# Optimization experiments

Measured on AMD Instinct MI355X. Metric: run time of the kernel, lower is better.

## Reference

```python
import jax, jax.numpy as jnp
import numpy as np

EPS = 1e-12  # matches torch F.normalize eps


def _l2_normalize(x, axis=-1):
    # torch.F.normalize: x / max(||x||, eps)
    n = jnp.sqrt(jnp.sum(x * x, axis=axis, keepdims=True))
    return x / jnp.maximum(n, EPS)


def setup_inputs() -> dict:
    N, n_classes, embed_dim = 32768, 1000, 1024
    key = jax.random.key(0)
    k_feat, k_lab, k_proto = jax.random.split(key, 3)

    features = jax.random.normal(k_feat, (N, embed_dim), dtype=jnp.float32)

    # one-hot float labels, as expected by `torch.matmul(labels, self.mean_class)`
    y = jax.random.randint(k_lab, (N,), 0, n_classes)
    labels = jax.nn.one_hot(y, n_classes, dtype=jnp.float32)

    # predefined prototypes: orthonormal rows (ortho_group.rvs equivalent via QR)
    g = jax.random.normal(k_proto, (embed_dim, embed_dim), dtype=jnp.float32)
    q, _ = jnp.linalg.qr(g)
    mean_class = q[:n_classes]  # [n_classes, embed_dim], orthonormal rows

    return {"features": features, "labels": labels, "mean_class": mean_class}


def reference(features, labels, mean_class):
    # features: [N, D]; labels: [N, C] one-hot; mean_class: [C, D]
    # (3-D feature mean-pooling branch not exercised: inputs are 2-D)
    proto_y = labels @ mean_class                 # [N, D]
    f = _l2_normalize(features, axis=1)
    p = _l2_normalize(proto_y, axis=1)
    # diag(f @ p.T) == rowwise dot product -> same math, O(N*D) not O(N^2*D)
    cos = jnp.einsum("nd,nd->n", f, p)            # [N]
    return jnp.mean(1.0 - cos)
```

## Files before the change

### kernel.cpp

```cpp
#include <hip/hip_runtime.h>

constexpr int N_CLASSES = 1000;
constexpr int EMBED     = 1024;

typedef float floatx4 __attribute__((ext_vector_type(4)));

__device__ __forceinline__ floatx4 ntload(const floatx4* p) {
    return __builtin_nontemporal_load(p);
}

__global__ __launch_bounds__(256, 4) void angular_pipelined_kernel(
    const float* __restrict__ features,
    const float* __restrict__ labels,
    const float* __restrict__ mean_class,
    float* __restrict__ partials,
    int n_rows)
{
    const int tid  = threadIdx.x;
    const int lane = tid & 63;
    const int wave = tid >> 6;
    const int wave_id = (blockIdx.x * blockDim.x + tid) >> 6;
    const int n_waves = (gridDim.x * blockDim.x) >> 6;

    float acc = 0.0f;

    int r = wave_id;
    floatx4 f0, f1, f2, f3, l0, l1, l2, l3;
    if (r < n_rows) {
        const floatx4* frow = (const floatx4*)(features + (size_t)r * EMBED);
        f0 = ntload(frow + lane);       f1 = ntload(frow + lane + 64);
        f2 = ntload(frow + lane + 128); f3 = ntload(frow + lane + 192);
        const floatx4* lrow = (const floatx4*)(labels + (size_t)r * N_CLASSES);
        l0 = ntload(lrow + lane);       l1 = ntload(lrow + lane + 64);
        l2 = ntload(lrow + lane + 128);
        l3 = (lane < N_CLASSES / 4 - 192) ? ntload(lrow + lane + 192)
                                          : (floatx4){0.f, 0.f, 0.f, 0.f};
    }

    while (r < n_rows) {
        const int rn = r + n_waves;
        const bool has_next = rn < n_rows;
        floatx4 nf0, nf1, nf2, nf3, nl0, nl1, nl2, nl3;
        if (has_next) {
            const floatx4* frow = (const floatx4*)(features + (size_t)rn * EMBED);
            nf0 = ntload(frow + lane);       nf1 = ntload(frow + lane + 64);
            nf2 = ntload(frow + lane + 128); nf3 = ntload(frow + lane + 192);
            const floatx4* lrow = (const floatx4*)(labels + (size_t)rn * N_CLASSES);
            nl0 = ntload(lrow + lane);       nl1 = ntload(lrow + lane + 64);
            nl2 = ntload(lrow + lane + 128);
            nl3 = (lane < N_CLASSES / 4 - 192) ? ntload(lrow + lane + 192)
                                               : (floatx4){0.f, 0.f, 0.f, 0.f};
        }

        int cand = -1;
        #define SCAN(V, IDX) { \
            if (V.x != 0.f || V.y != 0.f || V.z != 0.f || V.w != 0.f) { \
                int c_ = 4 * (IDX); \
                if      (V.y != 0.f) c_ += 1; \
                else if (V.z != 0.f) c_ += 2; \
                else if (V.w != 0.f) c_ += 3; \
                cand = c_; \
            } }
        SCAN(l0, lane) SCAN(l1, lane + 64) SCAN(l2, lane + 128) SCAN(l3, lane + 192)
        #undef SCAN

        unsigned long long m = __ballot(cand >= 0);
        int cls = __shfl(cand, __ffsll(m) - 1, 64);
        cls = __builtin_amdgcn_readfirstlane(cls);

        const floatx4* prow = (const floatx4*)(mean_class + (size_t)cls * EMBED);
        floatx4 p0 = prow[lane];
        floatx4 p1 = prow[lane + 64];
        floatx4 p2 = prow[lane + 128];
        floatx4 p3 = prow[lane + 192];

        float ff = 0.f, pp = 0.f, fp = 0.f;
        #define DOT3(F, P) \
            ff += F.x*F.x + F.y*F.y + F.z*F.z + F.w*F.w; \
            pp += P.x*P.x + P.y*P.y + P.z*P.z + P.w*P.w; \
            fp += F.x*P.x + F.y*P.y + F.z*P.z + F.w*P.w;
        DOT3(f0, p0) DOT3(f1, p1) DOT3(f2, p2) DOT3(f3, p3)
        #undef DOT3

        #pragma unroll
        for (int msk = 1; msk < 64; msk <<= 1) {
            ff += __shfl_xor(ff, msk, 64);
            pp += __shfl_xor(pp, msk, 64);
            fp += __shfl_xor(fp, msk, 64);
        }
        acc += 1.0f - fp / (fmaxf(sqrtf(ff), 1e-12f) * fmaxf(sqrtf(pp), 1e-12f));

        r = rn;
        if (has_next) {
            f0 = nf0; f1 = nf1; f2 = nf2; f3 = nf3;
            l0 = nl0; l1 = nl1; l2 = nl2; l3 = nl3;
        }
    }

    __shared__ float s_red[4];
    if (lane == 0) s_red[wave] = acc;
    __syncthreads();
    if (tid == 0)
        partials[blockIdx.x] = s_red[0] + s_red[1] + s_red[2] + s_red[3];
}

__global__ __launch_bounds__(256) void reduce_partials_kernel(
    const float* __restrict__ partials, int num_partials,
    float* __restrict__ out, float inv_n)
{
    const int tid  = threadIdx.x;
    const int lane = tid & 63;
    const int wave = tid >> 6;
    __shared__ float s_red[4];

    float acc = 0.0f;
    for (int i = tid; i < num_partials; i += 256)
        acc += partials[i];
    #pragma unroll
    for (int msk = 1; msk < 64; msk <<= 1)
        acc += __shfl_xor(acc, msk, 64);
    if (lane == 0) s_red[wave] = acc;
    __syncthreads();
    if (tid == 0)
        out[0] = (s_red[0] + s_red[1] + s_red[2] + s_red[3]) * inv_n;
}

extern "C" void kernel_launch(void* const* d_in, const int* in_sizes, int n_in,
                              void* d_out, int out_size, void* d_ws, size_t ws_size,
                              hipStream_t stream) {
    const float* features   = (const float*)d_in[0];
    const float* labels     = (const float*)d_in[1];
    const float* mean_class = (const float*)d_in[2];
    float* out = (float*)d_out;
    float* partials = (float*)d_ws;

    const int n_rows = in_sizes[0] / EMBED;
    const int num_blocks = 1024;

    angular_pipelined_kernel<<<num_blocks, 256, 0, stream>>>(
        features, labels, mean_class, partials, n_rows);
    reduce_partials_kernel<<<1, 256, 0, stream>>>(
        partials, num_blocks, out, 1.0f / (float)n_rows);
}
```

Measured before the change: 256.0 us.

## Split label scan into separate kernel and simplify feature dot pass

```diff
diff --git a/kernel.cpp b/kernel.cpp
--- a/kernel.cpp
+++ b/kernel.cpp
@@ -9,12 +9,43 @@
     return __builtin_nontemporal_load(p);
 }
 
-__global__ __launch_bounds__(256, 4) void angular_pipelined_kernel(
+__global__ __launch_bounds__(256, 8) void label_scan_kernel(
+    const float* __restrict__ labels,
+    int* __restrict__ cls_arr, int n_rows)
+{
+    const int tid  = threadIdx.x;
+    const int lane = tid & 63;
+    const int wave_id = (blockIdx.x * blockDim.x + tid) >> 6;
+    const int n_waves = (gridDim.x * blockDim.x) >> 6;
+
+    const float wb = (float)(4 * lane + 1);
+    const floatx4 w0 = {wb,          wb + 1.f,   wb + 2.f,   wb + 3.f};
+    const floatx4 w1 = {wb + 256.f,  wb + 257.f, wb + 258.f, wb + 259.f};
+    const floatx4 w2 = {wb + 512.f,  wb + 513.f, wb + 514.f, wb + 515.f};
+    const floatx4 w3 = {wb + 768.f,  wb + 769.f, wb + 770.f, wb + 771.f};
+
+    for (int r = wave_id; r < n_rows; r += n_waves) {
+        const floatx4* lr = (const floatx4*)(labels + (size_t)r * N_CLASSES);
+        floatx4 l0 = ntload(lr + lane);
+        floatx4 l1 = ntload(lr + lane + 64);
+        floatx4 l2 = ntload(lr + lane + 128);
+        floatx4 l3 = (lane < N_CLASSES / 4 - 192) ? ntload(lr + lane + 192)
+                                                  : (floatx4){0.f, 0.f, 0.f, 0.f};
+        float c = l0.x*w0.x + l0.y*w0.y + l0.z*w0.z + l0.w*w0.w;
+        c += l1.x*w1.x + l1.y*w1.y + l1.z*w1.z + l1.w*w1.w;
+        c += l2.x*w2.x + l2.y*w2.y + l2.z*w2.z + l2.w*w2.w;
+        c += l3.x*w3.x + l3.y*w3.y + l3.z*w3.z + l3.w*w3.w;
+        unsigned long long m = __ballot(c != 0.0f);
+        float cf = __shfl(c, __ffsll(m) - 1, 64);
+        if (lane == 0) cls_arr[r] = (int)cf - 1;
+    }
+}
+
+__global__ __launch_bounds__(256, 8) void feature_dot_kernel(
     const float* __restrict__ features,
-    const float* __restrict__ labels,
     const float* __restrict__ mean_class,
-    float* __restrict__ partials,
-    int n_rows)
+    const int* __restrict__ cls_arr,
+    float* __restrict__ partials, int n_rows)
 {
     const int tid  = threadIdx.x;
     const int lane = tid & 63;
@@ -25,76 +56,48 @@
     float acc = 0.0f;
 
     int r = wave_id;
-    floatx4 f0, f1, f2, f3, l0, l1, l2, l3;
-    if (r < n_rows) {
-        const floatx4* frow = (const floatx4*)(features + (size_t)r * EMBED);
-        f0 = ntload(frow + lane);       f1 = ntload(frow + lane + 64);
-        f2 = ntload(frow + lane + 128); f3 = ntload(frow + lane + 192);
-        const floatx4* lrow = (const floatx4*)(labels + (size_t)r * N_CLASSES);
-        l0 = ntload(lrow + lane);       l1 = ntload(lrow + lane + 64);
-        l2 = ntload(lrow + lane + 128);
-        l3 = (lane < N_CLASSES / 4 - 192) ? ntload(lrow + lane + 192)
-                                          : (floatx4){0.f, 0.f, 0.f, 0.f};
-    }
+    int cls_cur = (r < n_rows) ? cls_arr[r] : 0;
 
-    while (r < n_rows) {
+    for (; r < n_rows; r += n_waves) {
         const int rn = r + n_waves;
-        const bool has_next = rn < n_rows;
-        floatx4 nf0, nf1, nf2, nf3, nl0, nl1, nl2, nl3;
-        if (has_next) {
-            const floatx4* frow = (const floatx4*)(features + (size_t)rn * EMBED);
-            nf0 = ntload(frow + lane);       nf1 = ntload(frow + lane + 64);
-            nf2 = ntload(frow + lane + 128); nf3 = ntload(frow + lane + 192);
-            const floatx4* lrow = (const floatx4*)(labels + (size_t)rn * N_CLASSES);
-            nl0 = ntload(lrow + lane);       nl1 = ntload(lrow + lane + 64);
-            nl2 = ntload(lrow + lane + 128);
-            nl3 = (lane < N_CLASSES / 4 - 192) ? ntload(lrow + lane + 192)
-                                               : (floatx4){0.f, 0.f, 0.f, 0.f};
-        }
 
-        int cand = -1;
-        #define SCAN(V, IDX) { \
-            if (V.x != 0.f || V.y != 0.f || V.z != 0.f || V.w != 0.f) { \
-                int c_ = 4 * (IDX); \
-                if      (V.y != 0.f) c_ += 1; \
-                else if (V.z != 0.f) c_ += 2; \
-                else if (V.w != 0.f) c_ += 3; \
-                cand = c_; \
-            } }
-        SCAN(l0, lane) SCAN(l1, lane + 64) SCAN(l2, lane + 128) SCAN(l3, lane + 192)
-        #undef SCAN
+        const floatx4* fr = (const floatx4*)(features + (size_t)r * EMBED);
+        floatx4 f0 = ntload(fr + lane);
+        floatx4 f1 = ntload(fr + lane + 64);
+        floatx4 f2 = ntload(fr + lane + 128);
+        floatx4 f3 = ntload(fr + lane + 192);
 
-        unsigned long long m = __ballot(cand >= 0);
-        int cls = __shfl(cand, __ffsll(m) - 1, 64);
-        cls = __builtin_amdgcn_readfirstlane(cls);
+        const int c = __builtin_amdgcn_readfirstlane(cls_cur);
+        const floatx4* pr = (const floatx4*)(mean_class + (size_t)c * EMBED);
+        floatx4 p0 = pr[lane];
+        floatx4 p1 = pr[lane + 64];
+        floatx4 p2 = pr[lane + 128];
+        floatx4 p3 = pr[lane + 192];
 
-        const floatx4* prow = (const floatx4*)(mean_class + (size_t)cls * EMBED);
-        floatx4 p0 = prow[lane];
-        floatx4 p1 = prow[lane + 64];
-        floatx4 p2 = prow[lane + 128];
-        floatx4 p3 = prow[lane + 192];
+        int cls_nxt = (rn < n_rows) ? cls_arr[rn] : 0;
 
         float ff = 0.f, pp = 0.f, fp = 0.f;
-        #define DOT3(F, P) \
-            ff += F.x*F.x + F.y*F.y + F.z*F.z + F.w*F.w; \
-            pp += P.x*P.x + P.y*P.y + P.z*P.z + P.w*P.w; \
-            fp += F.x*P.x + F.y*P.y + F.z*P.z + F.w*P.w;
-        DOT3(f0, p0) DOT3(f1, p1) DOT3(f2, p2) DOT3(f3, p3)
-        #undef DOT3
-
+        ff += f0.x*f0.x + f0.y*f0.y + f0.z*f0.z + f0.w*f0.w;
+        pp += p0.x*p0.x + p0.y*p0.y + p0.z*p0.z + p0.w*p0.w;
+        fp += f0.x*p0.x + f0.y*p0.y + f0.z*p0.z + f0.w*p0.w;
+        ff += f1.x*f1.x + f1.y*f1.y + f1.z*f1.z + f1.w*f1.w;
+        pp += p1.x*p1.x + p1.y*p1.y + p1.z*p1.z + p1.w*p1.w;
+        fp += f1.x*p1.x + f1.y*p1.y + f1.z*p1.z + f1.w*p1.w;
+        ff += f2.x*f2.x + f2.y*f2.y + f2.z*f2.z + f2.w*f2.w;
+        pp += p2.x*p2.x + p2.y*p2.y + p2.z*p2.z + p2.w*p2.w;
+        fp += f2.x*p2.x + f2.y*p2.y + f2.z*p2.z + f2.w*p2.w;
+        ff += f3.x*f3.x + f3.y*f3.y + f3.z*f3.z + f3.w*f3.w;
+        pp += p3.x*p3.x + p3.y*p3.y + p3.z*p3.z + p3.w*p3.w;
+        fp += f3.x*p3.x + f3.y*p3.y + f3.z*p3.z + f3.w*p3.w;
         #pragma unroll
         for (int msk = 1; msk < 64; msk <<= 1) {
             ff += __shfl_xor(ff, msk, 64);
             pp += __shfl_xor(pp, msk, 64);
             fp += __shfl_xor(fp, msk, 64);
         }
-        acc += 1.0f - fp / (fmaxf(sqrtf(ff), 1e-12f) * fmaxf(sqrtf(pp), 1e-12f));
+        acc += 1.0f - fp * __builtin_amdgcn_rsqf(fmaxf(ff * pp, 1e-24f));
 
-        r = rn;
-        if (has_next) {
-            f0 = nf0; f1 = nf1; f2 = nf2; f3 = nf3;
-            l0 = nl0; l1 = nl1; l2 = nl2; l3 = nl3;
-        }
+        cls_cur = cls_nxt;
     }
 
     __shared__ float s_red[4];
@@ -132,13 +135,16 @@
     const float* labels     = (const float*)d_in[1];
     const float* mean_class = (const float*)d_in[2];
     float* out = (float*)d_out;
+
     float* partials = (float*)d_ws;
+    int*   cls_arr  = (int*)((char*)d_ws + 16384);
 
     const int n_rows = in_sizes[0] / EMBED;
-    const int num_blocks = 1024;
+    const int num_blocks = 2048;
 
-    angular_pipelined_kernel<<<num_blocks, 256, 0, stream>>>(
-        features, labels, mean_class, partials, n_rows);
+    label_scan_kernel<<<num_blocks, 256, 0, stream>>>(labels, cls_arr, n_rows);
+    feature_dot_kernel<<<num_blocks, 256, 0, stream>>>(
+        features, mean_class, cls_arr, partials, n_rows);
     reduce_partials_kernel<<<1, 256, 0, stream>>>(
         partials, num_blocks, out, 1.0f / (float)n_rows);
 }
```

Result: no change. 258.9 us (+1.1%).
